# Performance work log

Hardware: AMD Instinct MI355X
Metric: run time of the kernel (lower is better)

The kernel has to match this reference:

```python
import jax, jax.numpy as jnp
import numpy as np

DT = 1e-3            # norse default integration step
TAU_MEM_INV = 50.0   # 1 / tau_mem, tau_mem = 0.02 from config
TAU_SYN_INV = 200.0  # norse default
V_TH = 1.0           # config['threshold']
ALPHA = 100.0        # SuperSpike surrogate sharpness (norse default)


@jax.custom_vjp
def spike(x):
    # Heaviside forward, SuperSpike surrogate gradient backward
    return (x > 0).astype(x.dtype)

def _spike_fwd(x):
    return (x > 0).astype(x.dtype), x

def _spike_bwd(res, g):
    return (g / (ALPHA * jnp.abs(res) + 1.0) ** 2,)

spike.defvjp(_spike_fwd, _spike_bwd)


def lif_step(v, i, inp):
    # norse lif_feed_forward_step: decay v and i, spike, reset, inject input into i
    v_dec = v + DT * TAU_MEM_INV * (-v + i)   # v_leak = 0
    i_dec = i - DT * TAU_SYN_INV * i
    s = spike(v_dec - V_TH)
    v_new = (1.0 - s) * v_dec                 # v_reset = 0
    i_new = i_dec + inp
    return s, v_new, i_new


def setup_inputs() -> dict:
    key = jax.random.key(0)
    ks = jax.random.split(key, 7)
    B, T, H, OUT = 256, 32, 1024, 10
    IN = 2 * 34 * 34  # 2312
    x = jax.random.uniform(ks[0], (B, T, 2, 34, 34), dtype=jnp.float32)
    s_in = 1.0 / np.sqrt(IN)
    s_h = 1.0 / np.sqrt(H)
    W1 = jax.random.uniform(ks[1], (H, IN), jnp.float32, -s_in, s_in)
    b1 = jax.random.uniform(ks[2], (H,), jnp.float32, -s_in, s_in)
    W2 = jax.random.uniform(ks[3], (H, H), jnp.float32, -s_h, s_h)
    b2 = jax.random.uniform(ks[4], (H,), jnp.float32, -s_h, s_h)
    Wout = jax.random.uniform(ks[5], (OUT, H), jnp.float32, -s_h, s_h)
    bout = jax.random.uniform(ks[6], (OUT,), jnp.float32, -s_h, s_h)
    return {"x": x, "W1": W1, "b1": b1, "W2": W2, "b2": b2, "Wout": Wout, "bout": bout}


def reference(x, W1, b1, W2, b2, Wout, bout):
    B, T = x.shape[0], x.shape[1]
    xt = x.reshape(B, T, -1).transpose(1, 0, 2)  # (T, B, IN): permute + flatten
    H, OUT = W1.shape[0], Wout.shape[0]
    zH = jnp.zeros((B, H), x.dtype)
    zO = jnp.zeros((B, OUT), x.dtype)
    carry0 = (zH, zH, zH, zH, zO, zO)  # (v1, i1, v2, i2, v_out, i_out)

    def step(carry, x_t):
        v1, i1, v2, i2, vo, io = carry
        s1, v1, i1 = lif_step(v1, i1, x_t @ W1.T + b1)
        s2, v2, i2 = lif_step(v2, i2, s1 @ W2.T + b2)
        so, vo, io = lif_step(vo, io, s2 @ Wout.T + bout)
        return (v1, i1, v2, i2, vo, io), so

    _, spikes = jax.lax.scan(step, carry0, xt)  # (T, B, OUT)
    return spikes.sum(axis=0)  # rate decoding -> (B, OUT)
```

## Files before the change

kernel.cpp:

```cpp
#include <hip/hip_runtime.h>


#define TB 256
#define TT 32
#define TH 1024
#define TIN 2312
#define TOUT 10
#define TM (TT * TB)
#define KP1 2368

typedef _Float16 f16_t;
typedef f16_t f16x8 __attribute__((ext_vector_type(8)));
typedef f16_t f16x4 __attribute__((ext_vector_type(4)));
typedef float floatx4 __attribute__((ext_vector_type(4)));

__device__ __forceinline__ void split2h(float v, f16_t& a, f16_t& b) {
  a = (f16_t)v;
  b = (f16_t)(v - (float)a);
}

__global__ __launch_bounds__(256) void split_w1h(const float* __restrict__ W,
                                                 f16_t* __restrict__ P,
                                                 long plane, int K, int Kp) {
  int k4 = (blockIdx.x * 256 + threadIdx.x) * 4;
  if (k4 >= Kp) return;
  long r = blockIdx.y;
  float4 v = (k4 < K) ? *(const float4*)(W + r * (long)K + k4)
                      : float4{0.f, 0.f, 0.f, 0.f};
  float t[4] = {v.x, v.y, v.z, v.w};
  f16x4 a, b;
  #pragma unroll
  for (int e = 0; e < 4; ++e) {
    f16_t x, y;
    split2h(t[e], x, y);
    a[e] = x; b[e] = y;
  }
  long o = r * (long)Kp + k4;
  *(f16x4*)(P + o) = a;
  *(f16x4*)(P + plane + o) = b;
}

__global__ __launch_bounds__(512, 2) void snn_gemm1(
    const float* __restrict__ Af, long sT, long sB,
    const f16_t* __restrict__ Bp, long planeB, int Kp, int K,
    const float* __restrict__ bias, float* __restrict__ C, int N) {
  constexpr int LDW = 36;
  __shared__ f16_t As[2][128 * LDW];
  __shared__ f16_t Bs[2][256 * LDW];

  const int tid = threadIdx.x;
  const int wave = tid >> 6, lane = tid & 63;
  const int quad = lane >> 4, l16 = lane & 15;
  const int wm = (wave & 1) * 64, wn = (wave >> 1) * 64;
  const long m0 = (long)blockIdx.x * 128, n0 = (long)blockIdx.y * 256;

  floatx4 acc[4][4];
  #pragma unroll
  for (int i = 0; i < 4; ++i)
    #pragma unroll
    for (int j = 0; j < 4; ++j) acc[i][j] = (floatx4){0.f, 0.f, 0.f, 0.f};

  const int cr = tid >> 2;
  const int cs = (tid & 3) * 8;
  const int crB = tid >> 1;
  const int csB = (tid & 1) * 16;
  float4 xv[2];
  f16x8 bv[2][2];

  auto prefetch = [&](int kb) {
    const long rA = m0 + cr;
    const int k0 = kb + cs;
    const float* xr = Af + (rA >> 8) * sT + (rA & 255) * sB + k0;
    xv[0] = (k0 < K) ? *(const float4*)xr : float4{0.f, 0.f, 0.f, 0.f};
    xv[1] = (k0 + 4 < K) ? *(const float4*)(xr + 4)
                         : float4{0.f, 0.f, 0.f, 0.f};
    const int kB = kb + csB;
    #pragma unroll
    for (int q = 0; q < 2; ++q) {
      const f16_t* br = Bp + q * planeB + (n0 + crB) * (long)Kp + kB;
      bv[q][0] = *(const f16x8*)br;
      bv[q][1] = *(const f16x8*)(br + 8);
    }
  };

  auto commit = [&]() {
    const int off = cr * LDW + cs;
    f16x8 h0, h1;
    float t[8] = {xv[0].x, xv[0].y, xv[0].z, xv[0].w,
                  xv[1].x, xv[1].y, xv[1].z, xv[1].w};
    #pragma unroll
    for (int e = 0; e < 8; ++e) {
      f16_t a, b;
      split2h(t[e], a, b);
      h0[e] = a; h1[e] = b;
    }
    *(f16x8*)(&As[0][off]) = h0;
    *(f16x8*)(&As[1][off]) = h1;
    const int offB = crB * LDW + csB;
    #pragma unroll
    for (int q = 0; q < 2; ++q) {
      *(f16x8*)(&Bs[q][offB]) = bv[q][0];
      *(f16x8*)(&Bs[q][offB + 8]) = bv[q][1];
    }
  };

  const int numT = Kp / 32;
  prefetch(0);
  for (int kt = 0; kt < numT; ++kt) {
    __syncthreads();
    commit();
    const int kbn = (kt + 1 < numT) ? (kt + 1) * 32 : 0;
    prefetch(kbn);
    __syncthreads();

    f16x8 afr[2][4];
    #pragma unroll
    for (int pa = 0; pa < 2; ++pa)
      #pragma unroll
      for (int i = 0; i < 4; ++i)
        afr[pa][i] =
            *(const f16x8*)(&As[pa][(wm + i * 16 + l16) * LDW + quad * 8]);

    #pragma unroll
    for (int pb = 0; pb < 2; ++pb) {
      f16x8 bfr[4];
      #pragma unroll
      for (int j = 0; j < 4; ++j)
        bfr[j] =
            *(const f16x8*)(&Bs[pb][(wn + j * 16 + l16) * LDW + quad * 8]);
      const int pamax = 1 - pb;
      #pragma unroll
      for (int pa = 0; pa < 2; ++pa) {
        if (pa > pamax) break;
        #pragma unroll
        for (int i = 0; i < 4; ++i)
          #pragma unroll
          for (int j = 0; j < 4; ++j)
            acc[i][j] = __builtin_amdgcn_mfma_f32_16x16x32_f16(
                afr[pa][i], bfr[j], acc[i][j], 0, 0, 0);
      }
    }
  }

  #pragma unroll
  for (int j = 0; j < 4; ++j) {
    const long col = n0 + wn + j * 16 + l16;
    const float bvv = bias[col];
    #pragma unroll
    for (int i = 0; i < 4; ++i) {
      const long row0 = m0 + wm + i * 16 + quad * 4;
      #pragma unroll
      for (int g = 0; g < 4; ++g)
        C[(row0 + g) * (long)N + col] = acc[i][j][g] + bvv;
    }
  }
}

__global__ __launch_bounds__(512, 2) void snn_gemm2(
    const f16_t* __restrict__ Ab, long sT, long sB,
    const f16_t* __restrict__ Bp, long planeB, int Kp,
    const float* __restrict__ bias, float* __restrict__ C, int N) {
  constexpr int LDW = 36;
  __shared__ f16_t As[128 * LDW];
  __shared__ f16_t Bs[2][256 * LDW];

  const int tid = threadIdx.x;
  const int wave = tid >> 6, lane = tid & 63;
  const int quad = lane >> 4, l16 = lane & 15;
  const int wm = (wave & 1) * 64, wn = (wave >> 1) * 64;
  const long m0 = (long)blockIdx.x * 128, n0 = (long)blockIdx.y * 256;

  floatx4 acc[4][4];
  #pragma unroll
  for (int i = 0; i < 4; ++i)
    #pragma unroll
    for (int j = 0; j < 4; ++j) acc[i][j] = (floatx4){0.f, 0.f, 0.f, 0.f};

  const int cr = tid >> 2;
  const int cs = (tid & 3) * 8;
  const int crB = tid >> 1;
  const int csB = (tid & 1) * 16;
  f16x8 av;
  f16x8 bv[2][2];

  auto prefetch = [&](int kb) {
    const long rA = m0 + cr;
    av = *(const f16x8*)(Ab + (rA >> 8) * sT + (rA & 255) * sB + kb + cs);
    const int kB = kb + csB;
    #pragma unroll
    for (int q = 0; q < 2; ++q) {
      const f16_t* br = Bp + q * planeB + (n0 + crB) * (long)Kp + kB;
      bv[q][0] = *(const f16x8*)br;
      bv[q][1] = *(const f16x8*)(br + 8);
    }
  };

  auto commit = [&]() {
    *(f16x8*)(&As[cr * LDW + cs]) = av;
    const int offB = crB * LDW + csB;
    #pragma unroll
    for (int q = 0; q < 2; ++q) {
      *(f16x8*)(&Bs[q][offB]) = bv[q][0];
      *(f16x8*)(&Bs[q][offB + 8]) = bv[q][1];
    }
  };

  const int numT = Kp / 32;
  prefetch(0);
  for (int kt = 0; kt < numT; ++kt) {
    __syncthreads();
    commit();
    const int kbn = (kt + 1 < numT) ? (kt + 1) * 32 : 0;
    prefetch(kbn);
    __syncthreads();

    f16x8 afr[4];
    #pragma unroll
    for (int i = 0; i < 4; ++i)
      afr[i] = *(const f16x8*)(&As[(wm + i * 16 + l16) * LDW + quad * 8]);

    #pragma unroll
    for (int pb = 0; pb < 2; ++pb) {
      f16x8 bfr[4];
      #pragma unroll
      for (int j = 0; j < 4; ++j)
        bfr[j] =
            *(const f16x8*)(&Bs[pb][(wn + j * 16 + l16) * LDW + quad * 8]);
      #pragma unroll
      for (int i = 0; i < 4; ++i)
        #pragma unroll
        for (int j = 0; j < 4; ++j)
          acc[i][j] = __builtin_amdgcn_mfma_f32_16x16x32_f16(
              afr[i], bfr[j], acc[i][j], 0, 0, 0);
    }
  }

  #pragma unroll
  for (int j = 0; j < 4; ++j) {
    const long col = n0 + wn + j * 16 + l16;
    const float bvv = bias[col];
    #pragma unroll
    for (int i = 0; i < 4; ++i) {
      const long row0 = m0 + wm + i * 16 + quad * 4;
      #pragma unroll
      for (int g = 0; g < 4; ++g)
        C[(row0 + g) * (long)N + col] = acc[i][j][g] + bvv;
    }
  }
}

__global__ __launch_bounds__(256) void lif_scan_f16(const float* __restrict__ I,
                                                    f16_t* __restrict__ S) {
  int idx = blockIdx.x * 256 + threadIdx.x;
  float v = 0.f, cur = 0.f;
  #pragma unroll
  for (int t = 0; t < TT; ++t) {
    float inp = I[(long)t * (TB * TH) + idx];
    float vd = fmaf(0.05f, cur - v, v);
    float id = cur - 0.2f * cur;
    float s = (vd > 1.0f) ? 1.0f : 0.f;
    v = (1.0f - s) * vd;
    cur = id + inp;
    S[(long)t * (TB * TH) + idx] = (f16_t)s;
  }
}

__global__ __launch_bounds__(256) void gemm3_kernel(
    const f16_t* __restrict__ S2, const float* __restrict__ Wout,
    const float* __restrict__ bout, float* __restrict__ I3) {
  int wv = (blockIdx.x * blockDim.x + threadIdx.x) >> 6;
  int lane = threadIdx.x & 63;
  if (wv >= TM) return;
  const f16_t* srow = S2 + (long)wv * TH;
  float acc[TOUT];
  #pragma unroll
  for (int o = 0; o < TOUT; ++o) acc[o] = 0.f;
  for (int k = lane; k < TH; k += 64) {
    float s = (float)srow[k];
    #pragma unroll
    for (int o = 0; o < TOUT; ++o) acc[o] = fmaf(s, Wout[o * TH + k], acc[o]);
  }
  #pragma unroll
  for (int off = 32; off > 0; off >>= 1)
    #pragma unroll
    for (int o = 0; o < TOUT; ++o) acc[o] += __shfl_down(acc[o], off, 64);
  if (lane == 0) {
    #pragma unroll
    for (int o = 0; o < TOUT; ++o) I3[(long)wv * TOUT + o] = acc[o] + bout[o];
  }
}

__global__ __launch_bounds__(256) void scan_out(const float* __restrict__ I3,
                                                float* __restrict__ out) {
  int idx = blockIdx.x * blockDim.x + threadIdx.x;
  if (idx >= TB * TOUT) return;
  float v = 0.f, cur = 0.f, cnt = 0.f;
  #pragma unroll
  for (int t = 0; t < TT; ++t) {
    float inp = I3[(long)t * (TB * TOUT) + idx];
    float vd = fmaf(0.05f, cur - v, v);
    float id = cur - 0.2f * cur;
    float s = (vd > 1.0f) ? 1.0f : 0.f;
    v = (1.0f - s) * vd;
    cur = id + inp;
    cnt += s;
  }
  out[idx] = cnt;
}

extern "C" void kernel_launch(void* const* d_in, const int* in_sizes, int n_in,
                              void* d_out, int out_size, void* d_ws,
                              size_t ws_size, hipStream_t stream) {
  const float* x    = (const float*)d_in[0];
  const float* W1   = (const float*)d_in[1];
  const float* b1   = (const float*)d_in[2];
  const float* W2   = (const float*)d_in[3];
  const float* b2   = (const float*)d_in[4];
  const float* Wout = (const float*)d_in[5];
  const float* bout = (const float*)d_in[6];

  char* base = (char*)d_ws;
  const long S2_BYTES = (long)TM * TH * 2;
  f16_t* W1p  = (f16_t*)base;
  f16_t* W2p  = (f16_t*)(base + 2L * TH * KP1 * 2);
  float* bufI = (float*)(base + S2_BYTES);
  f16_t* S1   = (f16_t*)(base + S2_BYTES + (long)TM * TH * 4);
  float* buf3 = (float*)(base + S2_BYTES + (long)TM * TH * 4 + (long)TM * TH * 2);
  f16_t* S2   = (f16_t*)base;

  split_w1h<<<dim3(3, TH), 256, 0, stream>>>(W1, W1p, (long)TH * KP1, TIN, KP1);
  split_w1h<<<dim3(1, TH), 256, 0, stream>>>(W2, W2p, (long)TH * TH, TH, TH);

  snn_gemm1<<<dim3(TM / 128, TH / 256), 512, 0, stream>>>(
      x, (long)TIN, (long)TT * TIN, W1p, (long)TH * KP1, KP1, TIN, b1, bufI,
      TH);

  lif_scan_f16<<<(TB * TH) / 256, 256, 0, stream>>>(bufI, S1);

  snn_gemm2<<<dim3(TM / 128, TH / 256), 512, 0, stream>>>(
      S1, (long)TB * TH, (long)TH, W2p, (long)TH * TH, TH, b2, bufI, TH);

  lif_scan_f16<<<(TB * TH) / 256, 256, 0, stream>>>(bufI, S2);

  gemm3_kernel<<<(TM * 64) / 256, 256, 0, stream>>>(S2, Wout, bout, buf3);

  scan_out<<<(TB * TOUT + 255) / 256, 256, 0, stream>>>(buf3, (float*)d_out);
}
```

Before: 332.0 us.

## Pre-swizzle weights into MFMA fragment layout and load B directly to registers

Weight split kernels now write W1/W2 hi/lo planes in per-wave MFMA fragment order, so each lane loads its B operand with one contiguous 16-byte global load. This removes the B tile from shared memory and its store/load traffic. B fragments are double-buffered in registers across k-steps. Block tiles shrink from 128x256 with 512 threads to 128x128 with 256 threads on a flattened grid. The trade-off is more register pressure and exposed global-load latency on B, with less B reuse per block.

```diff
diff --git a/kernel.cpp b/kernel.cpp
--- a/kernel.cpp
+++ b/kernel.cpp
@@ -7,11 +7,11 @@
 #define TIN 2312
 #define TOUT 10
 #define TM (TT * TB)
-#define KP1 2368
+#define NK1 74
+#define NK2 32
 
 typedef _Float16 f16_t;
 typedef f16_t f16x8 __attribute__((ext_vector_type(8)));
-typedef f16_t f16x4 __attribute__((ext_vector_type(4)));
 typedef float floatx4 __attribute__((ext_vector_type(4)));
 
 __device__ __forceinline__ void split2h(float v, f16_t& a, f16_t& b) {
@@ -19,40 +19,49 @@
   b = (f16_t)(v - (float)a);
 }
 
-__global__ __launch_bounds__(256) void split_w1h(const float* __restrict__ W,
-                                                 f16_t* __restrict__ P,
-                                                 long plane, int K, int Kp) {
-  int k4 = (blockIdx.x * 256 + threadIdx.x) * 4;
-  if (k4 >= Kp) return;
-  long r = blockIdx.y;
-  float4 v = (k4 < K) ? *(const float4*)(W + r * (long)K + k4)
-                      : float4{0.f, 0.f, 0.f, 0.f};
-  float t[4] = {v.x, v.y, v.z, v.w};
-  f16x4 a, b;
-  #pragma unroll
-  for (int e = 0; e < 4; ++e) {
-    f16_t x, y;
-    split2h(t[e], x, y);
-    a[e] = x; b[e] = y;
-  }
-  long o = r * (long)Kp + k4;
-  *(f16x4*)(P + o) = a;
-  *(f16x4*)(P + plane + o) = b;
-}
-
-__global__ __launch_bounds__(512, 2) void snn_gemm1(
+__global__ __launch_bounds__(256) void split_w_frag(
+    const float* __restrict__ W, f16_t* __restrict__ P, long plane,
+    int K, int nk32) {
+  const int fid = blockIdx.x * 4 + (threadIdx.x >> 6);
+  const int lane = threadIdx.x & 63;
+  const int n16 = fid / nk32, k32 = fid - n16 * nk32;
+  const long row = n16 * 16 + (lane & 15);
+  const int k0 = k32 * 32 + (lane >> 4) * 8;
+  float t[8];
+  if (k0 + 8 <= K) {
+    float4 v0 = *(const float4*)(W + row * K + k0);
+    float4 v1 = *(const float4*)(W + row * K + k0 + 4);
+    t[0] = v0.x; t[1] = v0.y; t[2] = v0.z; t[3] = v0.w;
+    t[4] = v1.x; t[5] = v1.y; t[6] = v1.z; t[7] = v1.w;
+  } else {
+    #pragma unroll
+    for (int e = 0; e < 8; ++e) t[e] = 0.f;
+  }
+  f16x8 h0, h1;
+  #pragma unroll
+  for (int e = 0; e < 8; ++e) {
+    f16_t a, b;
+    split2h(t[e], a, b);
+    h0[e] = a; h1[e] = b;
+  }
+  const long o = (long)fid * 512 + lane * 8;
+  *(f16x8*)(P + o) = h0;
+  *(f16x8*)(P + plane + o) = h1;
+}
+
+__global__ __launch_bounds__(256, 2) void snn_gemm1(
     const float* __restrict__ Af, long sT, long sB,
-    const f16_t* __restrict__ Bp, long planeB, int Kp, int K,
+    const f16_t* __restrict__ Bf, long planeB, int nk32, int K,
     const float* __restrict__ bias, float* __restrict__ C, int N) {
   constexpr int LDW = 36;
   __shared__ f16_t As[2][128 * LDW];
-  __shared__ f16_t Bs[2][256 * LDW];
 
   const int tid = threadIdx.x;
   const int wave = tid >> 6, lane = tid & 63;
   const int quad = lane >> 4, l16 = lane & 15;
   const int wm = (wave & 1) * 64, wn = (wave >> 1) * 64;
-  const long m0 = (long)blockIdx.x * 128, n0 = (long)blockIdx.y * 256;
+  const int mblk = blockIdx.x >> 3, nblk = blockIdx.x & 7;
+  const long m0 = (long)mblk * 128, n0 = (long)nblk * 128;
 
   floatx4 acc[4][4];
   #pragma unroll
@@ -60,58 +69,60 @@
     #pragma unroll
     for (int j = 0; j < 4; ++j) acc[i][j] = (floatx4){0.f, 0.f, 0.f, 0.f};
 
-  const int cr = tid >> 2;
-  const int cs = (tid & 3) * 8;
-  const int crB = tid >> 1;
-  const int csB = (tid & 1) * 16;
-  float4 xv[2];
-  f16x8 bv[2][2];
-
-  auto prefetch = [&](int kb) {
+  const int cr = tid >> 1;
+  const int cs = (tid & 1) * 16;
+  float4 xv[4];
+
+  const f16_t* Bw = Bf + (((n0 + wn) >> 4) * (long)nk32) * 512 + lane * 8;
+
+  auto prefetchA = [&](int kb) {
     const long rA = m0 + cr;
     const int k0 = kb + cs;
     const float* xr = Af + (rA >> 8) * sT + (rA & 255) * sB + k0;
-    xv[0] = (k0 < K) ? *(const float4*)xr : float4{0.f, 0.f, 0.f, 0.f};
-    xv[1] = (k0 + 4 < K) ? *(const float4*)(xr + 4)
-                         : float4{0.f, 0.f, 0.f, 0.f};
-    const int kB = kb + csB;
-    #pragma unroll
-    for (int q = 0; q < 2; ++q) {
-      const f16_t* br = Bp + q * planeB + (n0 + crB) * (long)Kp + kB;
-      bv[q][0] = *(const f16x8*)br;
-      bv[q][1] = *(const f16x8*)(br + 8);
+    #pragma unroll
+    for (int u = 0; u < 4; ++u)
+      xv[u] = (k0 + u * 4 < K) ? *(const float4*)(xr + u * 4)
+                               : float4{0.f, 0.f, 0.f, 0.f};
+  };
+
+  auto commitA = [&]() {
+    const int off = cr * LDW + cs;
+    #pragma unroll
+    for (int h = 0; h < 2; ++h) {
+      float t[8] = {xv[2 * h].x,     xv[2 * h].y,     xv[2 * h].z,
+                    xv[2 * h].w,     xv[2 * h + 1].x, xv[2 * h + 1].y,
+                    xv[2 * h + 1].z, xv[2 * h + 1].w};
+      f16x8 a8, b8;
+      #pragma unroll
+      for (int e = 0; e < 8; ++e) {
+        f16_t a, b;
+        split2h(t[e], a, b);
+        a8[e] = a; b8[e] = b;
+      }
+      *(f16x8*)(&As[0][off + h * 8]) = a8;
+      *(f16x8*)(&As[1][off + h * 8]) = b8;
     }
   };
 
-  auto commit = [&]() {
-    const int off = cr * LDW + cs;
-    f16x8 h0, h1;
-    float t[8] = {xv[0].x, xv[0].y, xv[0].z, xv[0].w,
-                  xv[1].x, xv[1].y, xv[1].z, xv[1].w};
-    #pragma unroll
-    for (int e = 0; e < 8; ++e) {
-      f16_t a, b;
-      split2h(t[e], a, b);
-      h0[e] = a; h1[e] = b;
-    }
-    *(f16x8*)(&As[0][off]) = h0;
-    *(f16x8*)(&As[1][off]) = h1;
-    const int offB = crB * LDW + csB;
-    #pragma unroll
-    for (int q = 0; q < 2; ++q) {
-      *(f16x8*)(&Bs[q][offB]) = bv[q][0];
-      *(f16x8*)(&Bs[q][offB + 8]) = bv[q][1];
-    }
-  };
-
-  const int numT = Kp / 32;
-  prefetch(0);
-  for (int kt = 0; kt < numT; ++kt) {
+  auto loadB = [&](int k32, f16x8 (&bf)[2][4]) {
+    #pragma unroll
+    for (int q = 0; q < 2; ++q)
+      #pragma unroll
+      for (int j = 0; j < 4; ++j)
+        bf[q][j] = *(const f16x8*)(Bw + q * planeB +
+                                   ((long)j * nk32 + k32) * 512);
+  };
+
+  f16x8 b0[2][4], b1[2][4];
+  prefetchA(0);
+  loadB(0, b0);
+
+  auto body = [&](int kt, f16x8 (&bc)[2][4], f16x8 (&bn)[2][4]) {
     __syncthreads();
-    commit();
-    const int kbn = (kt + 1 < numT) ? (kt + 1) * 32 : 0;
-    prefetch(kbn);
+    commitA();
+    prefetchA(kt + 1 < nk32 ? (kt + 1) * 32 : 0);
     __syncthreads();
+    loadB(kt + 1 < nk32 ? kt + 1 : 0, bn);
 
     f16x8 afr[2][4];
     #pragma unroll
@@ -123,11 +134,6 @@
 
     #pragma unroll
     for (int pb = 0; pb < 2; ++pb) {
-      f16x8 bfr[4];
-      #pragma unroll
-      for (int j = 0; j < 4; ++j)
-        bfr[j] =
-            *(const f16x8*)(&Bs[pb][(wn + j * 16 + l16) * LDW + quad * 8]);
       const int pamax = 1 - pb;
       #pragma unroll
       for (int pa = 0; pa < 2; ++pa) {
@@ -137,9 +143,14 @@
           #pragma unroll
           for (int j = 0; j < 4; ++j)
             acc[i][j] = __builtin_amdgcn_mfma_f32_16x16x32_f16(
-                afr[pa][i], bfr[j], acc[i][j], 0, 0, 0);
+                afr[pa][i], bc[pb][j], acc[i][j], 0, 0, 0);
       }
     }
+  };
+
+  for (int kt = 0; kt < nk32; kt += 2) {
+    body(kt, b0, b1);
+    body(kt + 1, b1, b0);
   }
 
   #pragma unroll
@@ -156,19 +167,19 @@
   }
 }
 
-__global__ __launch_bounds__(512, 2) void snn_gemm2(
+__global__ __launch_bounds__(256, 2) void snn_gemm2(
     const f16_t* __restrict__ Ab, long sT, long sB,
-    const f16_t* __restrict__ Bp, long planeB, int Kp,
+    const f16_t* __restrict__ Bf, long planeB, int nk32,
     const float* __restrict__ bias, float* __restrict__ C, int N) {
   constexpr int LDW = 36;
   __shared__ f16_t As[128 * LDW];
-  __shared__ f16_t Bs[2][256 * LDW];
 
   const int tid = threadIdx.x;
   const int wave = tid >> 6, lane = tid & 63;
   const int quad = lane >> 4, l16 = lane & 15;
   const int wm = (wave & 1) * 64, wn = (wave >> 1) * 64;
-  const long m0 = (long)blockIdx.x * 128, n0 = (long)blockIdx.y * 256;
+  const int mblk = blockIdx.x >> 3, nblk = blockIdx.x & 7;
+  const long m0 = (long)mblk * 128, n0 = (long)nblk * 128;
 
   floatx4 acc[4][4];
   #pragma unroll
@@ -176,43 +187,44 @@
     #pragma unroll
     for (int j = 0; j < 4; ++j) acc[i][j] = (floatx4){0.f, 0.f, 0.f, 0.f};
 
-  const int cr = tid >> 2;
-  const int cs = (tid & 3) * 8;
-  const int crB = tid >> 1;
-  const int csB = (tid & 1) * 16;
-  f16x8 av;
-  f16x8 bv[2][2];
-
-  auto prefetch = [&](int kb) {
+  const int cr = tid >> 1;
+  const int cs = (tid & 1) * 16;
+  f16x8 av[2];
+
+  const f16_t* Bw = Bf + (((n0 + wn) >> 4) * (long)nk32) * 512 + lane * 8;
+
+  auto prefetchA = [&](int kb) {
     const long rA = m0 + cr;
-    av = *(const f16x8*)(Ab + (rA >> 8) * sT + (rA & 255) * sB + kb + cs);
-    const int kB = kb + csB;
-    #pragma unroll
-    for (int q = 0; q < 2; ++q) {
-      const f16_t* br = Bp + q * planeB + (n0 + crB) * (long)Kp + kB;
-      bv[q][0] = *(const f16x8*)br;
-      bv[q][1] = *(const f16x8*)(br + 8);
-    }
-  };
-
-  auto commit = [&]() {
-    *(f16x8*)(&As[cr * LDW + cs]) = av;
-    const int offB = crB * LDW + csB;
-    #pragma unroll
-    for (int q = 0; q < 2; ++q) {
-      *(f16x8*)(&Bs[q][offB]) = bv[q][0];
-      *(f16x8*)(&Bs[q][offB + 8]) = bv[q][1];
-    }
-  };
-
-  const int numT = Kp / 32;
-  prefetch(0);
-  for (int kt = 0; kt < numT; ++kt) {
+    const f16_t* ar = Ab + (rA >> 8) * sT + (rA & 255) * sB + kb + cs;
+    av[0] = *(const f16x8*)ar;
+    av[1] = *(const f16x8*)(ar + 8);
+  };
+
+  auto commitA = [&]() {
+    const int off = cr * LDW + cs;
+    *(f16x8*)(&As[off]) = av[0];
+    *(f16x8*)(&As[off + 8]) = av[1];
+  };
+
+  auto loadB = [&](int k32, f16x8 (&bf)[2][4]) {
+    #pragma unroll
+    for (int q = 0; q < 2; ++q)
+      #pragma unroll
+      for (int j = 0; j < 4; ++j)
+        bf[q][j] = *(const f16x8*)(Bw + q * planeB +
+                                   ((long)j * nk32 + k32) * 512);
+  };
+
+  f16x8 b0[2][4], b1[2][4];
+  prefetchA(0);
+  loadB(0, b0);
+
+  auto body = [&](int kt, f16x8 (&bc)[2][4], f16x8 (&bn)[2][4]) {
     __syncthreads();
-    commit();
-    const int kbn = (kt + 1 < numT) ? (kt + 1) * 32 : 0;
-    prefetch(kbn);
+    commitA();
+    prefetchA(kt + 1 < nk32 ? (kt + 1) * 32 : 0);
     __syncthreads();
+    loadB(kt + 1 < nk32 ? kt + 1 : 0, bn);
 
     f16x8 afr[4];
     #pragma unroll
@@ -220,19 +232,18 @@
       afr[i] = *(const f16x8*)(&As[(wm + i * 16 + l16) * LDW + quad * 8]);
 
     #pragma unroll
-    for (int pb = 0; pb < 2; ++pb) {
-      f16x8 bfr[4];
-      #pragma unroll
-      for (int j = 0; j < 4; ++j)
-        bfr[j] =
-            *(const f16x8*)(&Bs[pb][(wn + j * 16 + l16) * LDW + quad * 8]);
+    for (int pb = 0; pb < 2; ++pb)
       #pragma unroll
       for (int i = 0; i < 4; ++i)
         #pragma unroll
         for (int j = 0; j < 4; ++j)
           acc[i][j] = __builtin_amdgcn_mfma_f32_16x16x32_f16(
-              afr[i], bfr[j], acc[i][j], 0, 0, 0);
-    }
+              afr[i], bc[pb][j], acc[i][j], 0, 0, 0);
+  };
+
+  for (int kt = 0; kt < nk32; kt += 2) {
+    body(kt, b0, b1);
+    body(kt + 1, b1, b0);
   }
 
   #pragma unroll
@@ -319,26 +330,28 @@
   const float* Wout = (const float*)d_in[5];
   const float* bout = (const float*)d_in[6];
 
+  const long PL1 = 64L * NK1 * 512;
+  const long PL2 = 64L * NK2 * 512;
+
   char* base = (char*)d_ws;
   const long S2_BYTES = (long)TM * TH * 2;
   f16_t* W1p  = (f16_t*)base;
-  f16_t* W2p  = (f16_t*)(base + 2L * TH * KP1 * 2);
+  f16_t* W2p  = (f16_t*)(base + 2 * PL1 * 2);
   float* bufI = (float*)(base + S2_BYTES);
   f16_t* S1   = (f16_t*)(base + S2_BYTES + (long)TM * TH * 4);
   float* buf3 = (float*)(base + S2_BYTES + (long)TM * TH * 4 + (long)TM * TH * 2);
   f16_t* S2   = (f16_t*)base;
 
-  split_w1h<<<dim3(3, TH), 256, 0, stream>>>(W1, W1p, (long)TH * KP1, TIN, KP1);
-  split_w1h<<<dim3(1, TH), 256, 0, stream>>>(W2, W2p, (long)TH * TH, TH, TH);
-
-  snn_gemm1<<<dim3(TM / 128, TH / 256), 512, 0, stream>>>(
-      x, (long)TIN, (long)TT * TIN, W1p, (long)TH * KP1, KP1, TIN, b1, bufI,
-      TH);
+  split_w_frag<<<64 * NK1 / 4, 256, 0, stream>>>(W1, W1p, PL1, TIN, NK1);
+  split_w_frag<<<64 * NK2 / 4, 256, 0, stream>>>(W2, W2p, PL2, TH, NK2);
+
+  snn_gemm1<<<512, 256, 0, stream>>>(x, (long)TIN, (long)TT * TIN, W1p, PL1,
+                                     NK1, TIN, b1, bufI, TH);
 
   lif_scan_f16<<<(TB * TH) / 256, 256, 0, stream>>>(bufI, S1);
 
-  snn_gemm2<<<dim3(TM / 128, TH / 256), 512, 0, stream>>>(
-      S1, (long)TB * TH, (long)TH, W2p, (long)TH * TH, TH, b2, bufI, TH);
+  snn_gemm2<<<512, 256, 0, stream>>>(S1, (long)TB * TH, (long)TH, W2p, PL2,
+                                     NK2, b2, bufI, TH);
 
   lif_scan_f16<<<(TB * TH) / 256, 256, 0, stream>>>(bufI, S2);
 
```

Result: slower. 350.8 us (+5.7%).

## Split-K the two hidden GEMMs with smaller N tiles and atomic accumulation

Applied to the files above, without the earlier changes.

Both hidden-layer GEMMs now use 128x128 output tiles instead of 128x256, and split K in two along gridDim.y. The grid grows from 256 to 1024 blocks, which is meant to fill the GPU better and raise occupancy. Partial sums are accumulated into C with atomicAdd, bias is added only by the first K-split, and the output buffer is zeroed with a memset before each GEMM. The cost is two extra memsets, twice the global atomic write traffic, and a launch_bounds minimum of 8 blocks that may squeeze registers.

```diff
diff --git a/kernel.cpp b/kernel.cpp
--- a/kernel.cpp
+++ b/kernel.cpp
@@ -8,6 +8,7 @@
 #define TOUT 10
 #define TM (TT * TB)
 #define KP1 2368
+#define LDW 36
 
 typedef _Float16 f16_t;
 typedef f16_t f16x8 __attribute__((ext_vector_type(8)));
@@ -40,47 +41,42 @@
   *(f16x4*)(P + plane + o) = b;
 }
 
-__global__ __launch_bounds__(512, 2) void snn_gemm1(
+__global__ __launch_bounds__(512, 8) void snn_gemm1(
     const float* __restrict__ Af, long sT, long sB,
     const f16_t* __restrict__ Bp, long planeB, int Kp, int K,
-    const float* __restrict__ bias, float* __restrict__ C, int N) {
-  constexpr int LDW = 36;
+    const float* __restrict__ bias, float* __restrict__ C, int N,
+    int tilesPerZ) {
   __shared__ f16_t As[2][128 * LDW];
-  __shared__ f16_t Bs[2][256 * LDW];
+  __shared__ f16_t Bs[2][128 * LDW];
 
   const int tid = threadIdx.x;
   const int wave = tid >> 6, lane = tid & 63;
   const int quad = lane >> 4, l16 = lane & 15;
-  const int wm = (wave & 1) * 64, wn = (wave >> 1) * 64;
-  const long m0 = (long)blockIdx.x * 128, n0 = (long)blockIdx.y * 256;
-
-  floatx4 acc[4][4];
-  #pragma unroll
-  for (int i = 0; i < 4; ++i)
+  const int wm = (wave & 3) * 32, wn = (wave >> 2) * 64;
+  const long m0 = (long)blockIdx.x * 128, n0 = (long)blockIdx.z * 128;
+  const int ktBase = blockIdx.y * tilesPerZ;
+
+  floatx4 acc[2][4];
+  #pragma unroll
+  for (int i = 0; i < 2; ++i)
     #pragma unroll
     for (int j = 0; j < 4; ++j) acc[i][j] = (floatx4){0.f, 0.f, 0.f, 0.f};
 
   const int cr = tid >> 2;
   const int cs = (tid & 3) * 8;
-  const int crB = tid >> 1;
-  const int csB = (tid & 1) * 16;
   float4 xv[2];
-  f16x8 bv[2][2];
-
-  auto prefetch = [&](int kb) {
-    const long rA = m0 + cr;
-    const int k0 = kb + cs;
-    const float* xr = Af + (rA >> 8) * sT + (rA & 255) * sB + k0;
-    xv[0] = (k0 < K) ? *(const float4*)xr : float4{0.f, 0.f, 0.f, 0.f};
-    xv[1] = (k0 + 4 < K) ? *(const float4*)(xr + 4)
+  f16x8 bv[2];
+  const float* xrow = Af + ((m0 + cr) >> 8) * sT + ((m0 + cr) & 255) * sB;
+  const f16_t* brow = Bp + (n0 + cr) * (long)Kp;
+
+  auto prefetch = [&](int kt) {
+    const int k0 = (ktBase + kt) * 32 + cs;
+    xv[0] = (k0 < K) ? *(const float4*)(xrow + k0) : float4{0.f, 0.f, 0.f, 0.f};
+    xv[1] = (k0 + 4 < K) ? *(const float4*)(xrow + k0 + 4)
                          : float4{0.f, 0.f, 0.f, 0.f};
-    const int kB = kb + csB;
-    #pragma unroll
-    for (int q = 0; q < 2; ++q) {
-      const f16_t* br = Bp + q * planeB + (n0 + crB) * (long)Kp + kB;
-      bv[q][0] = *(const f16x8*)br;
-      bv[q][1] = *(const f16x8*)(br + 8);
-    }
+    #pragma unroll
+    for (int q = 0; q < 2; ++q)
+      bv[q] = *(const f16x8*)(brow + q * planeB + k0);
   };
 
   auto commit = [&]() {
@@ -96,28 +92,22 @@
     }
     *(f16x8*)(&As[0][off]) = h0;
     *(f16x8*)(&As[1][off]) = h1;
-    const int offB = crB * LDW + csB;
-    #pragma unroll
-    for (int q = 0; q < 2; ++q) {
-      *(f16x8*)(&Bs[q][offB]) = bv[q][0];
-      *(f16x8*)(&Bs[q][offB + 8]) = bv[q][1];
-    }
+    #pragma unroll
+    for (int q = 0; q < 2; ++q) *(f16x8*)(&Bs[q][off]) = bv[q];
   };
 
-  const int numT = Kp / 32;
   prefetch(0);
-  for (int kt = 0; kt < numT; ++kt) {
+  for (int kt = 0; kt < tilesPerZ; ++kt) {
     __syncthreads();
     commit();
-    const int kbn = (kt + 1 < numT) ? (kt + 1) * 32 : 0;
-    prefetch(kbn);
+    prefetch(kt + 1 < tilesPerZ ? kt + 1 : 0);
     __syncthreads();
 
-    f16x8 afr[2][4];
+    f16x8 afr[2][2];
     #pragma unroll
     for (int pa = 0; pa < 2; ++pa)
       #pragma unroll
-      for (int i = 0; i < 4; ++i)
+      for (int i = 0; i < 2; ++i)
         afr[pa][i] =
             *(const f16x8*)(&As[pa][(wm + i * 16 + l16) * LDW + quad * 8]);
 
@@ -133,7 +123,7 @@
       for (int pa = 0; pa < 2; ++pa) {
         if (pa > pamax) break;
         #pragma unroll
-        for (int i = 0; i < 4; ++i)
+        for (int i = 0; i < 2; ++i)
           #pragma unroll
           for (int j = 0; j < 4; ++j)
             acc[i][j] = __builtin_amdgcn_mfma_f32_16x16x32_f16(
@@ -142,81 +132,74 @@
     }
   }
 
+  const bool first = (blockIdx.y == 0);
   #pragma unroll
   for (int j = 0; j < 4; ++j) {
     const long col = n0 + wn + j * 16 + l16;
-    const float bvv = bias[col];
-    #pragma unroll
-    for (int i = 0; i < 4; ++i) {
+    const float bvv = first ? bias[col] : 0.f;
+    #pragma unroll
+    for (int i = 0; i < 2; ++i) {
       const long row0 = m0 + wm + i * 16 + quad * 4;
       #pragma unroll
       for (int g = 0; g < 4; ++g)
-        C[(row0 + g) * (long)N + col] = acc[i][j][g] + bvv;
-    }
-  }
-}
-
-__global__ __launch_bounds__(512, 2) void snn_gemm2(
+        atomicAdd(&C[(row0 + g) * (long)N + col], acc[i][j][g] + bvv);
+    }
+  }
+}
+
+__global__ __launch_bounds__(512, 8) void snn_gemm2(
     const f16_t* __restrict__ Ab, long sT, long sB,
     const f16_t* __restrict__ Bp, long planeB, int Kp,
-    const float* __restrict__ bias, float* __restrict__ C, int N) {
-  constexpr int LDW = 36;
+    const float* __restrict__ bias, float* __restrict__ C, int N,
+    int tilesPerZ) {
   __shared__ f16_t As[128 * LDW];
-  __shared__ f16_t Bs[2][256 * LDW];
+  __shared__ f16_t Bs[2][128 * LDW];
 
   const int tid = threadIdx.x;
   const int wave = tid >> 6, lane = tid & 63;
   const int quad = lane >> 4, l16 = lane & 15;
-  const int wm = (wave & 1) * 64, wn = (wave >> 1) * 64;
-  const long m0 = (long)blockIdx.x * 128, n0 = (long)blockIdx.y * 256;
-
-  floatx4 acc[4][4];
-  #pragma unroll
-  for (int i = 0; i < 4; ++i)
+  const int wm = (wave & 3) * 32, wn = (wave >> 2) * 64;
+  const long m0 = (long)blockIdx.x * 128, n0 = (long)blockIdx.z * 128;
+  const int ktBase = blockIdx.y * tilesPerZ;
+
+  floatx4 acc[2][4];
+  #pragma unroll
+  for (int i = 0; i < 2; ++i)
     #pragma unroll
     for (int j = 0; j < 4; ++j) acc[i][j] = (floatx4){0.f, 0.f, 0.f, 0.f};
 
   const int cr = tid >> 2;
   const int cs = (tid & 3) * 8;
-  const int crB = tid >> 1;
-  const int csB = (tid & 1) * 16;
   f16x8 av;
-  f16x8 bv[2][2];
-
-  auto prefetch = [&](int kb) {
-    const long rA = m0 + cr;
-    av = *(const f16x8*)(Ab + (rA >> 8) * sT + (rA & 255) * sB + kb + cs);
-    const int kB = kb + csB;
-    #pragma unroll
-    for (int q = 0; q < 2; ++q) {
-      const f16_t* br = Bp + q * planeB + (n0 + crB) * (long)Kp + kB;
-      bv[q][0] = *(const f16x8*)br;
-      bv[q][1] = *(const f16x8*)(br + 8);
-    }
+  f16x8 bv[2];
+  const f16_t* arow = Ab + ((m0 + cr) >> 8) * sT + ((m0 + cr) & 255) * sB;
+  const f16_t* brow = Bp + (n0 + cr) * (long)Kp;
+
+  auto prefetch = [&](int kt) {
+    const int k0 = (ktBase + kt) * 32 + cs;
+    av = *(const f16x8*)(arow + k0);
+    #pragma unroll
+    for (int q = 0; q < 2; ++q)
+      bv[q] = *(const f16x8*)(brow + q * planeB + k0);
   };
 
   auto commit = [&]() {
-    *(f16x8*)(&As[cr * LDW + cs]) = av;
-    const int offB = crB * LDW + csB;
-    #pragma unroll
-    for (int q = 0; q < 2; ++q) {
-      *(f16x8*)(&Bs[q][offB]) = bv[q][0];
-      *(f16x8*)(&Bs[q][offB + 8]) = bv[q][1];
-    }
+    const int off = cr * LDW + cs;
+    *(f16x8*)(&As[off]) = av;
+    #pragma unroll
+    for (int q = 0; q < 2; ++q) *(f16x8*)(&Bs[q][off]) = bv[q];
   };
 
-  const int numT = Kp / 32;
   prefetch(0);
-  for (int kt = 0; kt < numT; ++kt) {
+  for (int kt = 0; kt < tilesPerZ; ++kt) {
     __syncthreads();
     commit();
-    const int kbn = (kt + 1 < numT) ? (kt + 1) * 32 : 0;
-    prefetch(kbn);
+    prefetch(kt + 1 < tilesPerZ ? kt + 1 : 0);
     __syncthreads();
 
-    f16x8 afr[4];
-    #pragma unroll
-    for (int i = 0; i < 4; ++i)
+    f16x8 afr[2];
+    #pragma unroll
+    for (int i = 0; i < 2; ++i)
       afr[i] = *(const f16x8*)(&As[(wm + i * 16 + l16) * LDW + quad * 8]);
 
     #pragma unroll
@@ -227,7 +210,7 @@
         bfr[j] =
             *(const f16x8*)(&Bs[pb][(wn + j * 16 + l16) * LDW + quad * 8]);
       #pragma unroll
-      for (int i = 0; i < 4; ++i)
+      for (int i = 0; i < 2; ++i)
         #pragma unroll
         for (int j = 0; j < 4; ++j)
           acc[i][j] = __builtin_amdgcn_mfma_f32_16x16x32_f16(
@@ -235,16 +218,17 @@
     }
   }
 
+  const bool first = (blockIdx.y == 0);
   #pragma unroll
   for (int j = 0; j < 4; ++j) {
     const long col = n0 + wn + j * 16 + l16;
-    const float bvv = bias[col];
-    #pragma unroll
-    for (int i = 0; i < 4; ++i) {
+    const float bvv = first ? bias[col] : 0.f;
+    #pragma unroll
+    for (int i = 0; i < 2; ++i) {
       const long row0 = m0 + wm + i * 16 + quad * 4;
       #pragma unroll
       for (int g = 0; g < 4; ++g)
-        C[(row0 + g) * (long)N + col] = acc[i][j][g] + bvv;
+        atomicAdd(&C[(row0 + g) * (long)N + col], acc[i][j][g] + bvv);
     }
   }
 }
@@ -331,14 +315,16 @@
   split_w1h<<<dim3(3, TH), 256, 0, stream>>>(W1, W1p, (long)TH * KP1, TIN, KP1);
   split_w1h<<<dim3(1, TH), 256, 0, stream>>>(W2, W2p, (long)TH * TH, TH, TH);
 
-  snn_gemm1<<<dim3(TM / 128, TH / 256), 512, 0, stream>>>(
+  hipMemsetAsync(bufI, 0, (long)TM * TH * 4, stream);
+  snn_gemm1<<<dim3(64, 2, 8), 512, 0, stream>>>(
       x, (long)TIN, (long)TT * TIN, W1p, (long)TH * KP1, KP1, TIN, b1, bufI,
-      TH);
+      TH, 37);
 
   lif_scan_f16<<<(TB * TH) / 256, 256, 0, stream>>>(bufI, S1);
 
-  snn_gemm2<<<dim3(TM / 128, TH / 256), 512, 0, stream>>>(
-      S1, (long)TB * TH, (long)TH, W2p, (long)TH * TH, TH, b2, bufI, TH);
+  hipMemsetAsync(bufI, 0, (long)TM * TH * 4, stream);
+  snn_gemm2<<<dim3(64, 2, 8), 512, 0, stream>>>(
+      S1, (long)TB * TH, (long)TH, W2p, (long)TH * TH, TH, b2, bufI, TH, 16);
 
   lif_scan_f16<<<(TB * TH) / 256, 256, 0, stream>>>(bufI, S2);
 
```

Measured after the change: 1.139 ms. 3.43x slower.
